# Performance work log

Hardware: AMD Instinct MI355X
Metric: run time of the kernel (lower is better)

The kernel has to match this reference:

```python
import jax, jax.numpy as jnp
import numpy as np

M, N, IN, H, NC = 2048, 64, 16, 256, 64
OUT = 3 * NC
NUM_LAYERS = 2


def _lstm_layer(x, Wih, Whh, bih, bhh):
    # x: (M, T, F); Wih: (4H, F); Whh: (4H, H). Torch gate order: i, f, g, o.
    xg = jnp.einsum('mtf,gf->mtg', x, Wih) + bih + bhh  # (M, T, 4H)
    h0 = jnp.zeros((x.shape[0], Whh.shape[1]), x.dtype)

    def step(carry, xt):
        h, c = carry
        gates = xt + h @ Whh.T
        i, f, g, o = jnp.split(gates, 4, axis=-1)
        c = jax.nn.sigmoid(f) * c + jax.nn.sigmoid(i) * jnp.tanh(g)
        h = jax.nn.sigmoid(o) * jnp.tanh(c)
        return (h, c), h

    (_, _), hs = jax.lax.scan(step, (h0, h0), jnp.swapaxes(xg, 0, 1))
    return jnp.swapaxes(hs, 0, 1)  # (M, T, H)


def setup_inputs() -> dict:
    key = jax.random.key(0)
    ks = jax.random.split(key, 12)
    s = 1.0 / np.sqrt(H)
    d = {
        'z': jax.random.normal(ks[0], (M, N, IN), jnp.float32),
        'Wih0': jax.random.normal(ks[1], (4 * H, IN), jnp.float32) * s,
        'Whh0': jax.random.normal(ks[2], (4 * H, H), jnp.float32) * s,
        'bih0': jax.random.normal(ks[3], (4 * H,), jnp.float32) * s,
        'bhh0': jax.random.normal(ks[4], (4 * H,), jnp.float32) * s,
        'Wih1': jax.random.normal(ks[5], (4 * H, H), jnp.float32) * s,
        'Whh1': jax.random.normal(ks[6], (4 * H, H), jnp.float32) * s,
        'bih1': jax.random.normal(ks[7], (4 * H,), jnp.float32) * s,
        'bhh1': jax.random.normal(ks[8], (4 * H,), jnp.float32) * s,
        'fcW': jax.random.normal(ks[9], (OUT, H), jnp.float32) * 0.02,
        'fcb': jax.random.normal(ks[10], (OUT,), jnp.float32) * 0.02,
    }
    return d


def reference(z, Wih0, Whh0, bih0, bhh0, Wih1, Whh1, bih1, bhh1, fcW, fcb):
    h = _lstm_layer(z, Wih0, Whh0, bih0, bhh0)
    h = _lstm_layer(h, Wih1, Whh1, bih1, bhh1)
    y = jnp.einsum('mth,oh->mto', h, fcW) + fcb  # (M, N, 3*NC)

    gammas = jax.nn.softmax(y[..., :NC], axis=2)
    sigmas = jnp.exp(y[..., NC:2 * NC])
    mus = y[..., 2 * NC:]

    key = jax.random.key(42)
    k1, k2 = jax.random.split(key)
    idx = jax.random.categorical(k1, jnp.log(gammas), axis=-1)  # (M, N)
    chosen_mu = jnp.take_along_axis(mus, idx[..., None], axis=2)     # (M, N, 1)
    chosen_sig = jnp.take_along_axis(sigmas, idx[..., None], axis=2)
    eps = jax.random.normal(k2, chosen_mu.shape, jnp.float32)
    x_pred = jax.lax.stop_gradient(chosen_mu + chosen_sig * eps)  # Normal.sample (no grad)

    kern_exp = (x_pred - mus) ** 2                         # broadcast repeat over NC
    kernels = jnp.exp(-0.5 * kern_exp) / sigmas ** 2
    kernels = kernels / ((2.0 * jnp.pi) ** (N / 2) * sigmas ** N)
    x_cond_prob = jnp.einsum('mtc,mtc->mt', gammas, kernels)  # (M, N)
    return x_pred, x_cond_prob
```

## Files before the change

kernel.cpp:

```cpp
#include <hip/hip_runtime.h>
#include <stdint.h>
#include <stddef.h>

#define Mdim 2048
#define Tdim 64
#define INdim 16
#define Hdim 256
#define NCdim 64
#define NUG 64
#define HSLAB (256 * 2048)
#define RSLOTS 16

typedef __attribute__((ext_vector_type(8))) short s16x8;
typedef __attribute__((ext_vector_type(4))) float f32x4;

#define PANEL_US (3 * 16 * 8 * 512)
#define SPOFF 65536
#define BFRAG_US (3 * 8 * 3 * 512)

#define OFF_BFRAG 0
#define OFF_WZ    1179648
#define OFF_BB    (OFF_WZ + 64 * 256)
#define OFF_WFCP  (OFF_BB + 64 * 32)
#define OFF_H0P   (OFF_WFCP + 256 * 64 * 4)
#define OFF_C0    (OFF_H0P + 1572864)
#define OFF_C1    (OFF_C0 + HSLAB)
#define OFF_RINGF (OFF_C1 + HSLAB)
#define OFF_Y     (OFF_RINGF + 12582912)
#define OFF_FCB3  (OFF_Y + RSLOTS * HSLAB)
#define WS_TOT    (OFF_FCB3 + 73728)

#define ROTL32(v, s) (((v) << (s)) | ((v) >> (32 - (s))))

__host__ __device__ inline void tf2x32(uint32_t k0, uint32_t k1, uint32_t x0, uint32_t x1,
                                       uint32_t* o0, uint32_t* o1) {
  uint32_t ks2 = k0 ^ k1 ^ 0x1BD11BDAu;
  x0 += k0; x1 += k1;
  x0 += x1; x1 = ROTL32(x1, 13); x1 ^= x0;
  x0 += x1; x1 = ROTL32(x1, 15); x1 ^= x0;
  x0 += x1; x1 = ROTL32(x1, 26); x1 ^= x0;
  x0 += x1; x1 = ROTL32(x1, 6);  x1 ^= x0;
  x0 += k1; x1 += ks2 + 1u;
  x0 += x1; x1 = ROTL32(x1, 17); x1 ^= x0;
  x0 += x1; x1 = ROTL32(x1, 29); x1 ^= x0;
  x0 += x1; x1 = ROTL32(x1, 16); x1 ^= x0;
  x0 += x1; x1 = ROTL32(x1, 24); x1 ^= x0;
  x0 += ks2; x1 += k0 + 2u;
  x0 += x1; x1 = ROTL32(x1, 13); x1 ^= x0;
  x0 += x1; x1 = ROTL32(x1, 15); x1 ^= x0;
  x0 += x1; x1 = ROTL32(x1, 26); x1 ^= x0;
  x0 += x1; x1 = ROTL32(x1, 6);  x1 ^= x0;
  x0 += k0; x1 += k1 + 3u;
  x0 += x1; x1 = ROTL32(x1, 17); x1 ^= x0;
  x0 += x1; x1 = ROTL32(x1, 29); x1 ^= x0;
  x0 += x1; x1 = ROTL32(x1, 16); x1 ^= x0;
  x0 += x1; x1 = ROTL32(x1, 24); x1 ^= x0;
  x0 += k1; x1 += ks2 + 4u;
  x0 += x1; x1 = ROTL32(x1, 13); x1 ^= x0;
  x0 += x1; x1 = ROTL32(x1, 15); x1 ^= x0;
  x0 += x1; x1 = ROTL32(x1, 26); x1 ^= x0;
  x0 += x1; x1 = ROTL32(x1, 6);  x1 ^= x0;
  x0 += ks2; x1 += k0 + 5u;
  *o0 = x0; *o1 = x1;
// ... 121 lines not shown
    unsigned short s2 = bf16_trunc(r1 - bf16_tof(s1));
    size_t base = ((size_t)(ug * 3 + cls) * 8 + kt) * (3 * 512) + pos;
    BF[base] = s0;
    BF[base + 512] = s1;
    BF[base + 1024] = s2;
  }
  for (int i = i0; i < 64 * 256; i += n) {
    int ug = i >> 8, k = (i >> 4) & 15, g = i & 15;
    int gd = (g & 3) * 256 + ug * 4 + (g >> 2);
    ws[OFF_WZ + i] = Wih0[gd * INdim + k];
  }
  for (int i = i0; i < 64 * 32; i += n) {
    int ug = i >> 5, r = i & 31, g = r & 15;
    int gd = (g & 3) * 256 + ug * 4 + (g >> 2);
    ws[OFF_BB + i] = (r < 16) ? (bih0[gd] + bhh0[gd]) : (bih1[gd] + bhh1[gd]);
  }
  unsigned short* BFC = (unsigned short*)(ws + OFF_FCB3);
  for (int i = i0; i < 12 * 8 * 512; i += n) {
    int ntkt = i >> 9, pos = i & 511;
    int nt = ntkt >> 3, kt = ntkt & 7;
    int l = pos >> 3, e = pos & 7;
    int c = nt * 16 + (l & 15);
    int k = kt * 32 + (l >> 4) * 8 + e;
    float w = fcW[c * Hdim + k];
    unsigned short s0 = bf16_trunc(w);
    float r1 = w - bf16_tof(s0);
    unsigned short s1 = bf16_trunc(r1);
    unsigned short s2 = bf16_trunc(r1 - bf16_tof(s1));
    size_t base = (size_t)ntkt * (3 * 512) + pos;
    BFC[base] = s0;
    BFC[base + 512] = s1;
    BFC[base + 1024] = s2;
  }
}

__device__ inline void cell1s(float gi, float gf, float gg, float go, float cold,
                              float* cn, float* hn) {
  float si = sigm_fast(gi), sf = sigm_fast(gf);
  float tg = fmaf(2.0f, sigm_fast(2.0f * gg), -1.0f);
  float so = sigm_fast(go);
  float cc = fmaf(sf, cold, si * tg);
  *cn = cc;
  *hn = so * fmaf(2.0f, sigm_fast(2.0f * cc), -1.0f);
}

#define GBS3 66

template <int MODE>
__launch_bounds__(512, 2)
__global__ void vfpg_step(const float* __restrict__ z, const float* __restrict__ ws,
                          float* __restrict__ wsm, int t) {
  __shared__ unsigned short lB01[2 * 2 * 8 * 2 * 512];
  __shared__ __align__(16) unsigned char uni[81920];
  __shared__ float lz[2 * 256];
  __shared__ float lbias[64];

  const int tid = threadIdx.x;
  const int rg = blockIdx.x & 7, ugc = blockIdx.x >> 3;
  const int mb = rg * 256;
  const int lane = tid & 63, wid = tid >> 6;
  float* gbuf = (float*)uni;

  {
    const unsigned short* BF = (const unsigned short*)(ws + OFF_BFRAG);
    const unsigned short* BG0 = BF + (size_t)(ugc * 2 + 0) * BFRAG_US;
    const unsigned short* BG1 = BF + (size_t)(ugc * 2 + 1) * BFRAG_US;
    for (int i = tid; i < 2 * 4608; i += 512) {
      int ugl = i / 4608;
      int r = i % 4608;
      int cls = r / 1536;
      int r2 = r % 1536;
      int kt = r2 / 192;
      int sp = (r2 / 64) % 3;
      int v = r2 & 63;
      const unsigned short* src = (ugl ? BG1 : BG0) + ((size_t)(cls * 8 + kt) * 3 + sp) * 512 + v * 8;
      s16x8 val = *(const s16x8*)src;
      if (cls < 2 && sp < 2) {
        ((s16x8*)lB01)[((((ugl * 2 + cls) * 8 + kt) * 2 + sp)) * 64 + v] = val;
      } else {
        int str = (cls == 2) ? (2 + sp) : cls;
        ((s16x8*)uni)[(((ugl * 5 + str) * 8 + kt)) * 64 + v] = val;
      }
    }
    if (tid < 128) ((float4*)lz)[tid] = ((const float4*)(ws + OFF_WZ + (ugc * 2) * 256))[tid];
    if (tid < 64) lbias[tid] = ws[OFF_BB + (ugc * 2) * 32 + tid];
  }
  __syncthreads();

  f32x4 aL0[2][2], aL1[2][2];
#pragma unroll
  for (int i = 0; i < 2; i++)
#pragma unroll
    for (int u = 0; u < 2; u++) { aL0[i][u] = (f32x4)0.0f; aL1[i][u] = (f32x4)0.0f; }

  if (MODE >= 1) {
    const unsigned short* p0 = (const unsigned short*)(ws + OFF_H0P) +
                               ((size_t)((t - 1) & 1) * 8 + rg) * PANEL_US;
    const unsigned short* p1 = (const unsigned short*)(ws + OFF_RINGF) +
                               ((size_t)((t - 2) & 15) * 8 + rg) * PANEL_US;
    const bool doH1 = (t >= 2);
    const s16x8* pL = (const s16x8*)lB01;
    const s16x8* pU = (const s16x8*)uni;

    s16x8 Ab0[6], Ab1[6];
    {
      size_t fb = ((size_t)(wid * 2) * 8 + 0) * 512 + lane * 8;
      Ab0[0] = *(const s16x8*)(p0 + fb);
      Ab0[1] = *(const s16x8*)(p0 + fb + SPOFF);
      Ab0[2] = *(const s16x8*)(p0 + fb + 2 * SPOFF);
      if (doH1) {
        Ab0[3] = *(const s16x8*)(p1 + fb);
        Ab0[4] = *(const s16x8*)(p1 + fb + SPOFF);
        Ab0[5] = *(const s16x8*)(p1 + fb + 2 * SPOFF);
      }
    }

#pragma unroll 1
    for (int kt = 0; kt < 8; kt++) {
      s16x8 bL0s0[2], bL0s1[2], bL0s2[2], bIs0[2], bIs1[2], bIs2[2], bHs0[2], bHs1[2], bHs2[2];
#pragma unroll
      for (int u = 0; u < 2; u++) {
        if (MODE == 1) {
          bL0s0[u] = pL[(((u * 2 + 0) * 8 + kt) * 2 + 0) * 64 + lane];
          bL0s1[u] = pL[(((u * 2 + 0) * 8 + kt) * 2 + 1) * 64 + lane];
          bL0s2[u] = pU[((u * 5 + 0) * 8 + kt) * 64 + lane];
        }
        bIs0[u] = pL[(((u * 2 + 1) * 8 + kt) * 2 + 0) * 64 + lane];
        bIs1[u] = pL[(((u * 2 + 1) * 8 + kt) * 2 + 1) * 64 + lane];
        bIs2[u] = pU[((u * 5 + 1) * 8 + kt) * 64 + lane];
        if (doH1) {
          bHs0[u] = pU[((u * 5 + 2) * 8 + kt) * 64 + lane];
          bHs1[u] = pU[((u * 5 + 3) * 8 + kt) * 64 + lane];
          bHs2[u] = pU[((u * 5 + 4) * 8 + kt) * 64 + lane];
        }
      }
#pragma unroll
      for (int i = 0; i < 2; i++) {
        s16x8* cur = (i & 1) ? Ab1 : Ab0;
        s16x8* nxt = (i & 1) ? Ab0 : Ab1;
        int nkt = (i < 1) ? kt : kt + 1;
        int ni = (i < 1) ? 1 : 0;
        if (nkt < 8) {
          size_t fb = ((size_t)(wid * 2 + ni) * 8 + nkt) * 512 + lane * 8;
          nxt[0] = *(const s16x8*)(p0 + fb);
          nxt[1] = *(const s16x8*)(p0 + fb + SPOFF);
          nxt[2] = *(const s16x8*)(p0 + fb + 2 * SPOFF);
          if (doH1) {
            nxt[3] = *(const s16x8*)(p1 + fb);
            nxt[4] = *(const s16x8*)(p1 + fb + SPOFF);
            nxt[5] = *(const s16x8*)(p1 + fb + 2 * SPOFF);
          }
        }
        s16x8 a0 = cur[0], a1 = cur[1], a2 = cur[2];
#pragma unroll
        for (int u = 0; u < 2; u++) {
          if (MODE == 1) {
            aL0[i][u] = __builtin_amdgcn_mfma_f32_16x16x32_bf16(a0, bL0s0[u], aL0[i][u], 0, 0, 0);
            aL0[i][u] = __builtin_amdgcn_mfma_f32_16x16x32_bf16(a0, bL0s1[u], aL0[i][u], 0, 0, 0);
            aL0[i][u] = __builtin_amdgcn_mfma_f32_16x16x32_bf16(a1, bL0s0[u], aL0[i][u], 0, 0, 0);
            aL0[i][u] = __builtin_amdgcn_mfma_f32_16x16x32_bf16(a1, bL0s1[u], aL0[i][u], 0, 0, 0);
            aL0[i][u] = __builtin_amdgcn_mfma_f32_16x16x32_bf16(a0, bL0s2[u], aL0[i][u], 0, 0, 0);
            aL0[i][u] = __builtin_amdgcn_mfma_f32_16x16x32_bf16(a2, bL0s0[u], aL0[i][u], 0, 0, 0);
          }
          aL1[i][u] = __builtin_amdgcn_mfma_f32_16x16x32_bf16(a0, bIs0[u], aL1[i][u], 0, 0, 0);
          aL1[i][u] = __builtin_amdgcn_mfma_f32_16x16x32_bf16(a0, bIs1[u], aL1[i][u], 0, 0, 0);
          aL1[i][u] = __builtin_amdgcn_mfma_f32_16x16x32_bf16(a1, bIs0[u], aL1[i][u], 0, 0, 0);
          aL1[i][u] = __builtin_amdgcn_mfma_f32_16x16x32_bf16(a1, bIs1[u], aL1[i][u], 0, 0, 0);
          aL1[i][u] = __builtin_amdgcn_mfma_f32_16x16x32_bf16(a0, bIs2[u], aL1[i][u], 0, 0, 0);
          aL1[i][u] = __builtin_amdgcn_mfma_f32_16x16x32_bf16(a2, bIs0[u], aL1[i][u], 0, 0, 0);
          if (doH1) {
            s16x8 c0 = cur[3], c1 = cur[4], c2 = cur[5];
            aL1[i][u] = __builtin_amdgcn_mfma_f32_16x16x32_bf16(c0, bHs0[u], aL1[i][u], 0, 0, 0);
            aL1[i][u] = __builtin_amdgcn_mfma_f32_16x16x32_bf16(c0, bHs1[u], aL1[i][u], 0, 0, 0);
            aL1[i][u] = __builtin_amdgcn_mfma_f32_16x16x32_bf16(c1, bHs0[u], aL1[i][u], 0, 0, 0);
            aL1[i][u] = __builtin_amdgcn_mfma_f32_16x16x32_bf16(c1, bHs1[u], aL1[i][u], 0, 0, 0);
            aL1[i][u] = __builtin_amdgcn_mfma_f32_16x16x32_bf16(c0, bHs2[u], aL1[i][u], 0, 0, 0);
            aL1[i][u] = __builtin_amdgcn_mfma_f32_16x16x32_bf16(c2, bHs0[u], aL1[i][u], 0, 0, 0);
          }
        }
      }
    }
  }
  __syncthreads();

  {
    int col = lane & 15, rb2 = (lane >> 4) * 4;
#pragma unroll
    for (int i = 0; i < 2; i++)
#pragma unroll
      for (int u = 0; u < 2; u++)
#pragma unroll
        for (int j = 0; j < 4; j++) {
          int row = (wid * 2 + i) * 16 + rb2 + j;
          if (MODE == 1) gbuf[row * GBS3 + u * 16 + col] = aL0[i][u][j];
          if (MODE >= 1) gbuf[row * GBS3 + 32 + u * 16 + col] = aL1[i][u][j];
        }
  }
  __syncthreads();

  float* c0w = wsm + OFF_C0;
  float* c1w = wsm + OFF_C1;
  const int ugl = tid >> 8;
  const int mloc = tid & 255;
  const int m = mb + mloc;
  const int ug = ugc * 2 + ugl;
  const int mtc = mloc >> 4, mrowc = mloc & 15;
  const int ktw = ug >> 3;
  const int lgw = (ug & 7) >> 1;
  const int ebase = (ug * 4) & 7;
  const int lww = lgw * 16 + mrowc;
  const size_t fo = ((size_t)mtc * 8 + ktw) * 512 + lww * 8 + ebase;

  if (MODE <= 1) {
    float zr[16];
#pragma unroll
    for (int f4 = 0; f4 < 4; f4++)
      *(float4*)&zr[f4 * 4] = *(const float4*)&z[(size_t)m * 1024 + t * 16 + f4 * 4];
    float g16[16];
#pragma unroll
    for (int gg = 0; gg < 16; gg++)
      g16[gg] = lbias[ugl * 32 + gg] + ((MODE == 1) ? gbuf[mloc * GBS3 + ugl * 16 + gg] : 0.0f);
    const float* lzu = lz + ugl * 256;
#pragma unroll
    for (int f = 0; f < 16; f++) {
      float zv = zr[f];
      float4 w0 = *(const float4*)&lzu[f * 16 + 0];
      float4 w1 = *(const float4*)&lzu[f * 16 + 4];
      float4 w2 = *(const float4*)&lzu[f * 16 + 8];
      float4 w3 = *(const float4*)&lzu[f * 16 + 12];
      g16[0] = fmaf(zv, w0.x, g16[0]);  g16[1] = fmaf(zv, w0.y, g16[1]);
      g16[2] = fmaf(zv, w0.z, g16[2]);  g16[3] = fmaf(zv, w0.w, g16[3]);
      g16[4] = fmaf(zv, w1.x, g16[4]);  g16[5] = fmaf(zv, w1.y, g16[5]);
      g16[6] = fmaf(zv, w1.z, g16[6]);  g16[7] = fmaf(zv, w1.w, g16[7]);
      g16[8] = fmaf(zv, w2.x, g16[8]);  g16[9] = fmaf(zv, w2.y, g16[9]);
      g16[10] = fmaf(zv, w2.z, g16[10]); g16[11] = fmaf(zv, w2.w, g16[11]);
      g16[12] = fmaf(zv, w3.x, g16[12]); g16[13] = fmaf(zv, w3.y, g16[13]);
      g16[14] = fmaf(zv, w3.z, g16[14]); g16[15] = fmaf(zv, w3.w, g16[15]);
    }
    unsigned short* wp = (unsigned short*)(wsm + OFF_H0P) +
                         ((size_t)(t & 1) * 8 + rg) * PANEL_US;
    short sp0[4], sp1[4], sp2[4];
#pragma unroll
    for (int ul = 0; ul < 4; ul++) {
      int u = ug * 4 + ul;
      size_t cidx = (size_t)u * 2048 + m;
      float cold = (MODE == 1) ? c0w[cidx] : 0.0f;
      float cn, hn;
      cell1s(g16[ul * 4 + 0], g16[ul * 4 + 1], g16[ul * 4 + 2], g16[ul * 4 + 3], cold, &cn, &hn);
      c0w[cidx] = cn;
      unsigned short s0 = bf16_trunc(hn);
      float r1 = hn - bf16_tof(s0);
      unsigned short s1 = bf16_trunc(r1);
      unsigned short s2 = bf16_trunc(r1 - bf16_tof(s1));
      sp0[ul] = (short)s0; sp1[ul] = (short)s1; sp2[ul] = (short)s2;
    }
    *(short4*)&wp[fo]             = make_short4(sp0[0], sp0[1], sp0[2], sp0[3]);
    *(short4*)&wp[fo + SPOFF]     = make_short4(sp1[0], sp1[1], sp1[2], sp1[3]);
    *(short4*)&wp[fo + 2 * SPOFF] = make_short4(sp2[0], sp2[1], sp2[2], sp2[3]);
  }

  if (MODE >= 1) {
    int slot = (t - 1) & 15;
    unsigned short* rp = (unsigned short*)(wsm + OFF_RINGF) +
                         ((size_t)slot * 8 + rg) * PANEL_US;
    short sp0[4], sp1[4], sp2[4];
#pragma unroll
    for (int ul = 0; ul < 4; ul++) {
      float gi = lbias[ugl * 32 + 16 + ul * 4 + 0] + gbuf[mloc * GBS3 + 32 + ugl * 16 + ul * 4 + 0];
      float gf = lbias[ugl * 32 + 16 + ul * 4 + 1] + gbuf[mloc * GBS3 + 32 + ugl * 16 + ul * 4 + 1];
      float gt = lbias[ugl * 32 + 16 + ul * 4 + 2] + gbuf[mloc * GBS3 + 32 + ugl * 16 + ul * 4 + 2];
      float go = lbias[ugl * 32 + 16 + ul * 4 + 3] + gbuf[mloc * GBS3 + 32 + ugl * 16 + ul * 4 + 3];
      int u = ug * 4 + ul;
      size_t cidx = (size_t)u * 2048 + m;
      float cold = (t >= 2) ? c1w[cidx] : 0.0f;
      float cn, hn;
      cell1s(gi, gf, gt, go, cold, &cn, &hn);
      c1w[cidx] = cn;
      unsigned short s0 = bf16_trunc(hn);
      float r1v = hn - bf16_tof(s0);
      unsigned short s1 = bf16_trunc(r1v);
      unsigned short s2 = bf16_trunc(r1v - bf16_tof(s1));
      sp0[ul] = (short)s0; sp1[ul] = (short)s1; sp2[ul] = (short)s2;
    }
    *(short4*)&rp[fo]             = make_short4(sp0[0], sp0[1], sp0[2], sp0[3]);
    *(short4*)&rp[fo + SPOFF]     = make_short4(sp1[0], sp1[1], sp1[2], sp1[3]);
    *(short4*)&rp[fo + 2 * SPOFF] = make_short4(sp2[0], sp2[1], sp2[2], sp2[3]);
  }
}

__launch_bounds__(512, 2)
__global__ void vfpg_fc(const float* __restrict__ ws, float* __restrict__ wsm) {
  const int tid = threadIdx.x;
  const int rg = blockIdx.x & 7;
  const int slot = (blockIdx.x >> 3) & 15;
  const int mtg = blockIdx.x >> 7;
  const int lane = tid & 63, wid = tid >> 6;
  const int mt = mtg * 8 + wid;

  const unsigned short* pa = (const unsigned short*)(ws + OFF_RINGF) +
                             ((size_t)slot * 8 + rg) * PANEL_US;
  const unsigned short* BFC = (const unsigned short*)(ws + OFF_FCB3);
  float* y = wsm + OFF_Y + (size_t)slot * (2048 * 192) + (size_t)(rg * 256) * 192;

  const int col = lane & 15, rb2 = (lane >> 4) * 4;

#pragma unroll 1
  for (int ng = 0; ng < 3; ng++) {
    f32x4 C[4];
#pragma unroll
    for (int j = 0; j < 4; j++) C[j] = (f32x4)0.0f;
#pragma unroll 1
    for (int kt = 0; kt < 8; kt++) {
      size_t fb = ((size_t)mt * 8 + kt) * 512 + lane * 8;
      s16x8 a0 = *(const s16x8*)(pa + fb);
      s16x8 a1 = *(const s16x8*)(pa + fb + SPOFF);
      s16x8 a2 = *(const s16x8*)(pa + fb + 2 * SPOFF);
#pragma unroll
      for (int n4 = 0; n4 < 4; n4++) {
        int nt = ng * 4 + n4;
        const unsigned short* bp = BFC + (size_t)(nt * 8 + kt) * (3 * 512) + lane * 8;
        s16x8 b0 = *(const s16x8*)(bp);
        s16x8 b1 = *(const s16x8*)(bp + 512);
        s16x8 b2 = *(const s16x8*)(bp + 1024);
        C[n4] = __builtin_amdgcn_mfma_f32_16x16x32_bf16(a0, b0, C[n4], 0, 0, 0);
        C[n4] = __builtin_amdgcn_mfma_f32_16x16x32_bf16(a0, b1, C[n4], 0, 0, 0);
        C[n4] = __builtin_amdgcn_mfma_f32_16x16x32_bf16(a1, b0, C[n4], 0, 0, 0);
        C[n4] = __builtin_amdgcn_mfma_f32_16x16x32_bf16(a1, b1, C[n4], 0, 0, 0);
        C[n4] = __builtin_amdgcn_mfma_f32_16x16x32_bf16(a0, b2, C[n4], 0, 0, 0);
        C[n4] = __builtin_amdgcn_mfma_f32_16x16x32_bf16(a2, b0, C[n4], 0, 0, 0);
      }
    }
#pragma unroll
    for (int n4 = 0; n4 < 4; n4++) {
      int c = (ng * 4 + n4) * 16 + col;
#pragma unroll
      for (int j = 0; j < 4; j++) {
        int mrow = mt * 16 + rb2 + j;
        y[(size_t)mrow * 192 + c] = C[n4][j];
      }
    }
  }
}

__launch_bounds__(512, 2)
__global__ void vfpg_samp(const float* __restrict__ ws, const float* __restrict__ fcb,
                          float* __restrict__ out, int tbase,
                          uint32_t k1a, uint32_t k1b, uint32_t k2a, uint32_t k2b) {
  const int tid = threadIdx.x;
  const int lane = tid & 63, wid = tid >> 6;
  const int ridx = blockIdx.x * 8 + wid;
  const int slot = ridx >> 11;
  const int m = ridx & 2047;

  const float* yrow = ws + OFF_Y + (size_t)ridx * 192;
  float yg = yrow[lane] + fcb[lane];
  float ys = yrow[64 + lane] + fcb[64 + lane];
  float ym = yrow[128 + lane] + fcb[128 + lane];

  uint32_t rid = (uint32_t)m * Tdim + (uint32_t)(tbase + slot);
  mdn_head(yg, ys, ym, lane, rid, k1a, k1b, k2a, k2b, out);
}

extern "C" void kernel_launch(void* const* d_in, const int* in_sizes, int n_in,
                              void* d_out, int out_size, void* d_ws, size_t ws_size,
                              hipStream_t stream) {
  const float* z    = (const float*)d_in[0];
  const float* Wih0 = (const float*)d_in[1];
  const float* Whh0 = (const float*)d_in[2];
  const float* bih0 = (const float*)d_in[3];
  const float* bhh0 = (const float*)d_in[4];
  const float* Wih1 = (const float*)d_in[5];
  const float* Whh1 = (const float*)d_in[6];
  const float* bih1 = (const float*)d_in[7];
  const float* bhh1 = (const float*)d_in[8];
  const float* fcW  = (const float*)d_in[9];
  const float* fcb  = (const float*)d_in[10];
  float* ws = (float*)d_ws;
  float* out = (float*)d_out;

  if (ws_size < (size_t)WS_TOT * sizeof(float)) return;

  vfpg_prep<<<dim3(512), dim3(256), 0, stream>>>(
      Wih0, Whh0, Wih1, Whh1, fcW, bih0, bhh0, bih1, bhh1, ws);

  uint32_t k1a, k1b, k2a, k2b;
  tf2x32(0u, 42u, 0u, 0u, &k1a, &k1b);
  tf2x32(0u, 42u, 0u, 1u, &k2a, &k2b);

  vfpg_step<0><<<dim3(256), dim3(512), 0, stream>>>(z, ws, ws, 0);
  for (int t = 1; t <= 63; t++) {
    vfpg_step<1><<<dim3(256), dim3(512), 0, stream>>>(z, ws, ws, t);
    if (t == 16 || t == 32 || t == 48) {
      vfpg_fc<<<dim3(256), dim3(512), 0, stream>>>(ws, ws);
      vfpg_samp<<<dim3(4096), dim3(512), 0, stream>>>(ws, fcb, out, t - 16,
                                                      k1a, k1b, k2a, k2b);
    }
  }
  vfpg_step<2><<<dim3(256), dim3(512), 0, stream>>>(z, ws, ws, 64);
  vfpg_fc<<<dim3(256), dim3(512), 0, stream>>>(ws, ws);
  vfpg_samp<<<dim3(4096), dim3(512), 0, stream>>>(ws, fcb, out, 48, k1a, k1b, k2a, k2b);
}
```

Measured before the change: 1.931 ms.

## Fuse per-timestep LSTM launches into one cooperative persistent kernel with barriers

Replaces the 65 step launches plus the periodic FC and sampling launches with one cooperative persistent kernel. It loops over all timesteps and synchronises each row group with an atomic-counter spin barrier in global memory. FC and the MDN head are folded into the step loop, and some weight fragments are now read from global memory each step instead of shared memory, freeing LDS. This removes launch overhead and per-launch LDS reloads, but adds spin-barrier cost, runs at one block per CU, and reads part of the B operands from cache instead of LDS.

After: 4.933 ms. 156% more time.

```diff
diff --git a/kernel.cpp b/kernel.cpp
--- a/kernel.cpp
+++ b/kernel.cpp
@@ -7,7 +7,6 @@
 #define INdim 16
 #define Hdim 256
 #define NCdim 64
-#define NUG 64
 #define HSLAB (256 * 2048)
 #define RSLOTS 16
 
@@ -28,7 +27,8 @@
 #define OFF_RINGF (OFF_C1 + HSLAB)
 #define OFF_Y     (OFF_RINGF + 12582912)
 #define OFF_FCB3  (OFF_Y + RSLOTS * HSLAB)
-#define WS_TOT    (OFF_FCB3 + 73728)
+#define OFF_SYNC  (OFF_FCB3 + 73728)
+#define WS_TOT    (OFF_SYNC + 128)
 
 #define ROTL32(v, s) (((v) << (s)) | ((v) >> (32 - (s))))
 
@@ -216,6 +216,7 @@
     BFC[base + 512] = s1;
     BFC[base + 1024] = s2;
   }
+  if (i0 < 128) ((unsigned int*)(ws + OFF_SYNC))[i0] = 0u;
 }
 
 __device__ inline void cell1s(float gi, float gf, float gg, float go, float cold,
@@ -230,12 +231,12 @@
 
 #define GBS3 66
 
-template <int MODE>
-__launch_bounds__(512, 2)
-__global__ void vfpg_step(const float* __restrict__ z, const float* __restrict__ ws,
-                          float* __restrict__ wsm, int t) {
+__launch_bounds__(512, 1)
+__global__ void vfpg_persist(const float* __restrict__ z, float* __restrict__ ws,
+                             const float* __restrict__ fcb, float* __restrict__ out,
+                             uint32_t k1a, uint32_t k1b, uint32_t k2a, uint32_t k2b) {
   __shared__ unsigned short lB01[2 * 2 * 8 * 2 * 512];
-  __shared__ __align__(16) unsigned char uni[81920];
+  __shared__ __align__(16) unsigned char uni[69632];
   __shared__ float lz[2 * 256];
   __shared__ float lbias[64];
 
@@ -244,305 +245,315 @@
   const int mb = rg * 256;
   const int lane = tid & 63, wid = tid >> 6;
   float* gbuf = (float*)uni;
-
-  {
-    const unsigned short* BF = (const unsigned short*)(ws + OFF_BFRAG);
-    const unsigned short* BG0 = BF + (size_t)(ugc * 2 + 0) * BFRAG_US;
-    const unsigned short* BG1 = BF + (size_t)(ugc * 2 + 1) * BFRAG_US;
-    for (int i = tid; i < 2 * 4608; i += 512) {
-      int ugl = i / 4608;
-      int r = i % 4608;
-      int cls = r / 1536;
-      int r2 = r % 1536;
-      int kt = r2 / 192;
-      int sp = (r2 / 64) % 3;
-      int v = r2 & 63;
-      const unsigned short* src = (ugl ? BG1 : BG0) + ((size_t)(cls * 8 + kt) * 3 + sp) * 512 + v * 8;
-      s16x8 val = *(const s16x8*)src;
-      if (cls < 2 && sp < 2) {
-        ((s16x8*)lB01)[((((ugl * 2 + cls) * 8 + kt) * 2 + sp)) * 64 + v] = val;
-      } else {
-        int str = (cls == 2) ? (2 + sp) : cls;
-        ((s16x8*)uni)[(((ugl * 5 + str) * 8 + kt)) * 64 + v] = val;
-      }
-    }
-    if (tid < 128) ((float4*)lz)[tid] = ((const float4*)(ws + OFF_WZ + (ugc * 2) * 256))[tid];
-    if (tid < 64) lbias[tid] = ws[OFF_BB + (ugc * 2) * 32 + tid];
-  }
+  unsigned int* sc = (unsigned int*)(ws + OFF_SYNC) + rg * 16;
+
+  const unsigned short* BF = (const unsigned short*)(ws + OFF_BFRAG);
+  const unsigned short* BG2[2] = {BF + (size_t)(ugc * 2 + 0) * BFRAG_US,
+                                  BF + (size_t)(ugc * 2 + 1) * BFRAG_US};
+
+  for (int i = tid; i < 2 * 2 * 8 * 2 * 64; i += 512) {
+    int ugl = i >> 11;
+    int r = i & 2047;
+    int cls = r >> 10;
+    int kt = (r >> 7) & 7;
+    int sp = (r >> 6) & 1;
+    int v = r & 63;
+    ((s16x8*)lB01)[(((ugl * 2 + cls) * 8 + kt) * 2 + sp) * 64 + v] =
+        *(const s16x8*)(BG2[ugl] + ((size_t)(cls * 8 + kt) * 3 + sp) * 512 + v * 8);
+  }
+  if (tid < 128) ((float4*)lz)[tid] = ((const float4*)(ws + OFF_WZ + (ugc * 2) * 256))[tid];
+  if (tid < 64) lbias[tid] = ws[OFF_BB + (ugc * 2) * 32 + tid];
   __syncthreads();
 
-  f32x4 aL0[2][2], aL1[2][2];
-#pragma unroll
-  for (int i = 0; i < 2; i++)
-#pragma unroll
-    for (int u = 0; u < 2; u++) { aL0[i][u] = (f32x4)0.0f; aL1[i][u] = (f32x4)0.0f; }
-
-  if (MODE >= 1) {
-    const unsigned short* p0 = (const unsigned short*)(ws + OFF_H0P) +
-                               ((size_t)((t - 1) & 1) * 8 + rg) * PANEL_US;
-    const unsigned short* p1 = (const unsigned short*)(ws + OFF_RINGF) +
-                               ((size_t)((t - 2) & 15) * 8 + rg) * PANEL_US;
+  float* c0w = ws + OFF_C0;
+  float* c1w = ws + OFF_C1;
+  const int ugl_c = tid >> 8;
+  const int mloc = tid & 255;
+  const int m = mb + mloc;
+  const int ug_c = ugc * 2 + ugl_c;
+  const int mtc = mloc >> 4, mrowc = mloc & 15;
+  const int ktw = ug_c >> 3;
+  const int lgw = (ug_c & 7) >> 1;
+  const int ebase = (ug_c * 4) & 7;
+  const int lww = lgw * 16 + mrowc;
+  const size_t fo = ((size_t)mtc * 8 + ktw) * 512 + lww * 8 + ebase;
+  const int fc_slot = ugc >> 1, fc_mhalf = ugc & 1;
+
+  unsigned int bcount = 0;
+
+#pragma unroll 1
+  for (int t = 0; t <= Tdim; t++) {
+    const bool doL0 = (t < Tdim);
+    const bool doL1 = (t >= 1);
     const bool doH1 = (t >= 2);
-    const s16x8* pL = (const s16x8*)lB01;
-    const s16x8* pU = (const s16x8*)uni;
-
-    s16x8 Ab0[6], Ab1[6];
-    {
-      size_t fb = ((size_t)(wid * 2) * 8 + 0) * 512 + lane * 8;
-      Ab0[0] = *(const s16x8*)(p0 + fb);
-      Ab0[1] = *(const s16x8*)(p0 + fb + SPOFF);
-      Ab0[2] = *(const s16x8*)(p0 + fb + 2 * SPOFF);
-      if (doH1) {
-        Ab0[3] = *(const s16x8*)(p1 + fb);
-        Ab0[4] = *(const s16x8*)(p1 + fb + SPOFF);
-        Ab0[5] = *(const s16x8*)(p1 + fb + 2 * SPOFF);
-      }
-    }
+
+    f32x4 aL0[2][2], aL1[2][2];
+#pragma unroll
+    for (int i = 0; i < 2; i++)
+#pragma unroll
+      for (int u = 0; u < 2; u++) { aL0[i][u] = (f32x4)0.0f; aL1[i][u] = (f32x4)0.0f; }
+
+    if (t >= 1) {
+      const unsigned short* p0 = (const unsigned short*)(ws + OFF_H0P) +
+                                 ((size_t)((t - 1) & 1) * 8 + rg) * PANEL_US;
+      const unsigned short* p1 = (const unsigned short*)(ws + OFF_RINGF) +
+                                 ((size_t)((t - 2) & 15) * 8 + rg) * PANEL_US;
+      const s16x8* pL = (const s16x8*)lB01;
+
+      s16x8 Ab0[6], Ab1[6];
+      {
+        size_t fb = ((size_t)(wid * 2) * 8 + 0) * 512 + lane * 8;
+        Ab0[0] = *(const s16x8*)(p0 + fb);
+        Ab0[1] = *(const s16x8*)(p0 + fb + SPOFF);
+        Ab0[2] = *(const s16x8*)(p0 + fb + 2 * SPOFF);
+        if (doH1) {
+          Ab0[3] = *(const s16x8*)(p1 + fb);
+          Ab0[4] = *(const s16x8*)(p1 + fb + SPOFF);
+          Ab0[5] = *(const s16x8*)(p1 + fb + 2 * SPOFF);
+        }
+      }
 
 #pragma unroll 1
-    for (int kt = 0; kt < 8; kt++) {
-      s16x8 bL0s0[2], bL0s1[2], bL0s2[2], bIs0[2], bIs1[2], bIs2[2], bHs0[2], bHs1[2], bHs2[2];
-#pragma unroll
-      for (int u = 0; u < 2; u++) {
-        if (MODE == 1) {
-          bL0s0[u] = pL[(((u * 2 + 0) * 8 + kt) * 2 + 0) * 64 + lane];
-          bL0s1[u] = pL[(((u * 2 + 0) * 8 + kt) * 2 + 1) * 64 + lane];
-          bL0s2[u] = pU[((u * 5 + 0) * 8 + kt) * 64 + lane];
-        }
-        bIs0[u] = pL[(((u * 2 + 1) * 8 + kt) * 2 + 0) * 64 + lane];
-        bIs1[u] = pL[(((u * 2 + 1) * 8 + kt) * 2 + 1) * 64 + lane];
-        bIs2[u] = pU[((u * 5 + 1) * 8 + kt) * 64 + lane];
-        if (doH1) {
-          bHs0[u] = pU[((u * 5 + 2) * 8 + kt) * 64 + lane];
-          bHs1[u] = pU[((u * 5 + 3) * 8 + kt) * 64 + lane];
-          bHs2[u] = pU[((u * 5 + 4) * 8 + kt) * 64 + lane];
-        }
-      }
-#pragma unroll
-      for (int i = 0; i < 2; i++) {
-        s16x8* cur = (i & 1) ? Ab1 : Ab0;
-        s16x8* nxt = (i & 1) ? Ab0 : Ab1;
-        int nkt = (i < 1) ? kt : kt + 1;
-        int ni = (i < 1) ? 1 : 0;
-        if (nkt < 8) {
-          size_t fb = ((size_t)(wid * 2 + ni) * 8 + nkt) * 512 + lane * 8;
-          nxt[0] = *(const s16x8*)(p0 + fb);
-          nxt[1] = *(const s16x8*)(p0 + fb + SPOFF);
-          nxt[2] = *(const s16x8*)(p0 + fb + 2 * SPOFF);
+      for (int kt = 0; kt < 8; kt++) {
+        s16x8 bL0s0[2], bL0s1[2], bL0s2[2], bIs0[2], bIs1[2], bIs2[2], bHs0[2], bHs1[2], bHs2[2];
+#pragma unroll
+        for (int u = 0; u < 2; u++) {
+          if (doL0) {
+            bL0s0[u] = pL[(((u * 2 + 0) * 8 + kt) * 2 + 0) * 64 + lane];
+            bL0s1[u] = pL[(((u * 2 + 0) * 8 + kt) * 2 + 1) * 64 + lane];
+            bL0s2[u] = *(const s16x8*)(BG2[u] + ((size_t)(0 * 8 + kt) * 3 + 2) * 512 + lane * 8);
+          }
+          bIs0[u] = pL[(((u * 2 + 1) * 8 + kt) * 2 + 0) * 64 + lane];
+          bIs1[u] = pL[(((u * 2 + 1) * 8 + kt) * 2 + 1) * 64 + lane];
+          bIs2[u] = *(const s16x8*)(BG2[u] + ((size_t)(1 * 8 + kt) * 3 + 2) * 512 + lane * 8);
           if (doH1) {
-            nxt[3] = *(const s16x8*)(p1 + fb);
-            nxt[4] = *(const s16x8*)(p1 + fb + SPOFF);
-            nxt[5] = *(const s16x8*)(p1 + fb + 2 * SPOFF);
+            bHs0[u] = *(const s16x8*)(BG2[u] + ((size_t)(2 * 8 + kt) * 3 + 0) * 512 + lane * 8);
+            bHs1[u] = *(const s16x8*)(BG2[u] + ((size_t)(2 * 8 + kt) * 3 + 1) * 512 + lane * 8);
+            bHs2[u] = *(const s16x8*)(BG2[u] + ((size_t)(2 * 8 + kt) * 3 + 2) * 512 + lane * 8);
           }
         }
-        s16x8 a0 = cur[0], a1 = cur[1], a2 = cur[2];
-#pragma unroll
-        for (int u = 0; u < 2; u++) {
-          if (MODE == 1) {
-            aL0[i][u] = __builtin_amdgcn_mfma_f32_16x16x32_bf16(a0, bL0s0[u], aL0[i][u], 0, 0, 0);
-            aL0[i][u] = __builtin_amdgcn_mfma_f32_16x16x32_bf16(a0, bL0s1[u], aL0[i][u], 0, 0, 0);
-            aL0[i][u] = __builtin_amdgcn_mfma_f32_16x16x32_bf16(a1, bL0s0[u], aL0[i][u], 0, 0, 0);
-            aL0[i][u] = __builtin_amdgcn_mfma_f32_16x16x32_bf16(a1, bL0s1[u], aL0[i][u], 0, 0, 0);
-            aL0[i][u] = __builtin_amdgcn_mfma_f32_16x16x32_bf16(a0, bL0s2[u], aL0[i][u], 0, 0, 0);
-            aL0[i][u] = __builtin_amdgcn_mfma_f32_16x16x32_bf16(a2, bL0s0[u], aL0[i][u], 0, 0, 0);
+#pragma unroll
+        for (int i = 0; i < 2; i++) {
+          s16x8* cur = (i & 1) ? Ab1 : Ab0;
+          s16x8* nxt = (i & 1) ? Ab0 : Ab1;
+          int nkt = (i < 1) ? kt : kt + 1;
+          int ni = (i < 1) ? 1 : 0;
+          if (nkt < 8) {
+            size_t fb = ((size_t)(wid * 2 + ni) * 8 + nkt) * 512 + lane * 8;
+            nxt[0] = *(const s16x8*)(p0 + fb);
+            nxt[1] = *(const s16x8*)(p0 + fb + SPOFF);
+            nxt[2] = *(const s16x8*)(p0 + fb + 2 * SPOFF);
+            if (doH1) {
+              nxt[3] = *(const s16x8*)(p1 + fb);
+              nxt[4] = *(const s16x8*)(p1 + fb + SPOFF);
+              nxt[5] = *(const s16x8*)(p1 + fb + 2 * SPOFF);
+            }
           }
-          aL1[i][u] = __builtin_amdgcn_mfma_f32_16x16x32_bf16(a0, bIs0[u], aL1[i][u], 0, 0, 0);
-          aL1[i][u] = __builtin_amdgcn_mfma_f32_16x16x32_bf16(a0, bIs1[u], aL1[i][u], 0, 0, 0);
-          aL1[i][u] = __builtin_amdgcn_mfma_f32_16x16x32_bf16(a1, bIs0[u], aL1[i][u], 0, 0, 0);
-          aL1[i][u] = __builtin_amdgcn_mfma_f32_16x16x32_bf16(a1, bIs1[u], aL1[i][u], 0, 0, 0);
-          aL1[i][u] = __builtin_amdgcn_mfma_f32_16x16x32_bf16(a0, bIs2[u], aL1[i][u], 0, 0, 0);
-          aL1[i][u] = __builtin_amdgcn_mfma_f32_16x16x32_bf16(a2, bIs0[u], aL1[i][u], 0, 0, 0);
-          if (doH1) {
-            s16x8 c0 = cur[3], c1 = cur[4], c2 = cur[5];
-            aL1[i][u] = __builtin_amdgcn_mfma_f32_16x16x32_bf16(c0, bHs0[u], aL1[i][u], 0, 0, 0);
-            aL1[i][u] = __builtin_amdgcn_mfma_f32_16x16x32_bf16(c0, bHs1[u], aL1[i][u], 0, 0, 0);
-            aL1[i][u] = __builtin_amdgcn_mfma_f32_16x16x32_bf16(c1, bHs0[u], aL1[i][u], 0, 0, 0);
-            aL1[i][u] = __builtin_amdgcn_mfma_f32_16x16x32_bf16(c1, bHs1[u], aL1[i][u], 0, 0, 0);
-            aL1[i][u] = __builtin_amdgcn_mfma_f32_16x16x32_bf16(c0, bHs2[u], aL1[i][u], 0, 0, 0);
-            aL1[i][u] = __builtin_amdgcn_mfma_f32_16x16x32_bf16(c2, bHs0[u], aL1[i][u], 0, 0, 0);
+          s16x8 a0 = cur[0], a1 = cur[1], a2 = cur[2];
+#pragma unroll
+          for (int u = 0; u < 2; u++) {
+            if (doL0) {
+              aL0[i][u] = __builtin_amdgcn_mfma_f32_16x16x32_bf16(a0, bL0s0[u], aL0[i][u], 0, 0, 0);
+              aL0[i][u] = __builtin_amdgcn_mfma_f32_16x16x32_bf16(a0, bL0s1[u], aL0[i][u], 0, 0, 0);
+              aL0[i][u] = __builtin_amdgcn_mfma_f32_16x16x32_bf16(a1, bL0s0[u], aL0[i][u], 0, 0, 0);
+              aL0[i][u] = __builtin_amdgcn_mfma_f32_16x16x32_bf16(a1, bL0s1[u], aL0[i][u], 0, 0, 0);
+              aL0[i][u] = __builtin_amdgcn_mfma_f32_16x16x32_bf16(a0, bL0s2[u], aL0[i][u], 0, 0, 0);
+              aL0[i][u] = __builtin_amdgcn_mfma_f32_16x16x32_bf16(a2, bL0s0[u], aL0[i][u], 0, 0, 0);
+            }
+            aL1[i][u] = __builtin_amdgcn_mfma_f32_16x16x32_bf16(a0, bIs0[u], aL1[i][u], 0, 0, 0);
+            aL1[i][u] = __builtin_amdgcn_mfma_f32_16x16x32_bf16(a0, bIs1[u], aL1[i][u], 0, 0, 0);
+            aL1[i][u] = __builtin_amdgcn_mfma_f32_16x16x32_bf16(a1, bIs0[u], aL1[i][u], 0, 0, 0);
+            aL1[i][u] = __builtin_amdgcn_mfma_f32_16x16x32_bf16(a1, bIs1[u], aL1[i][u], 0, 0, 0);
+            aL1[i][u] = __builtin_amdgcn_mfma_f32_16x16x32_bf16(a0, bIs2[u], aL1[i][u], 0, 0, 0);
+            aL1[i][u] = __builtin_amdgcn_mfma_f32_16x16x32_bf16(a2, bIs0[u], aL1[i][u], 0, 0, 0);
+            if (doH1) {
+              s16x8 c0 = cur[3], c1 = cur[4], c2 = cur[5];
+              aL1[i][u] = __builtin_amdgcn_mfma_f32_16x16x32_bf16(c0, bHs0[u], aL1[i][u], 0, 0, 0);
+              aL1[i][u] = __builtin_amdgcn_mfma_f32_16x16x32_bf16(c0, bHs1[u], aL1[i][u], 0, 0, 0);
+              aL1[i][u] = __builtin_amdgcn_mfma_f32_16x16x32_bf16(c1, bHs0[u], aL1[i][u], 0, 0, 0);
+              aL1[i][u] = __builtin_amdgcn_mfma_f32_16x16x32_bf16(c1, bHs1[u], aL1[i][u], 0, 0, 0);
+              aL1[i][u] = __builtin_amdgcn_mfma_f32_16x16x32_bf16(c0, bHs2[u], aL1[i][u], 0, 0, 0);
+              aL1[i][u] = __builtin_amdgcn_mfma_f32_16x16x32_bf16(c2, bHs0[u], aL1[i][u], 0, 0, 0);
+            }
           }
         }
       }
+
+      {
+        int col = lane & 15, rb2 = (lane >> 4) * 4;
+#pragma unroll
+        for (int i = 0; i < 2; i++)
+#pragma unroll
+          for (int u = 0; u < 2; u++)
+#pragma unroll
+            for (int j = 0; j < 4; j++) {
+              int row = (wid * 2 + i) * 16 + rb2 + j;
+              if (doL0) gbuf[row * GBS3 + u * 16 + col] = aL0[i][u][j];
+              gbuf[row * GBS3 + 32 + u * 16 + col] = aL1[i][u][j];
+            }
+      }
     }
-  }
-  __syncthreads();
-
-  {
-    int col = lane & 15, rb2 = (lane >> 4) * 4;
-#pragma unroll
-    for (int i = 0; i < 2; i++)
-#pragma unroll
-      for (int u = 0; u < 2; u++)
-#pragma unroll
-        for (int j = 0; j < 4; j++) {
-          int row = (wid * 2 + i) * 16 + rb2 + j;
-          if (MODE == 1) gbuf[row * GBS3 + u * 16 + col] = aL0[i][u][j];
-          if (MODE >= 1) gbuf[row * GBS3 + 32 + u * 16 + col] = aL1[i][u][j];
+    __syncthreads();
+
+    if (doL0) {
+      float zr[16];
+#pragma unroll
+      for (int f4 = 0; f4 < 4; f4++)
+        *(float4*)&zr[f4 * 4] = *(const float4*)&z[(size_t)m * 1024 + t * 16 + f4 * 4];
+      float g16[16];
+#pragma unroll
+      for (int gg = 0; gg < 16; gg++)
+        g16[gg] = lbias[ugl_c * 32 + gg] + ((t >= 1) ? gbuf[mloc * GBS3 + ugl_c * 16 + gg] : 0.0f);
+      const float* lzu = lz + ugl_c * 256;
+#pragma unroll
+      for (int f = 0; f < 16; f++) {
+        float zv = zr[f];
+        float4 w0 = *(const float4*)&lzu[f * 16 + 0];
+        float4 w1 = *(const float4*)&lzu[f * 16 + 4];
+        float4 w2 = *(const float4*)&lzu[f * 16 + 8];
+        float4 w3 = *(const float4*)&lzu[f * 16 + 12];
+        g16[0] = fmaf(zv, w0.x, g16[0]);  g16[1] = fmaf(zv, w0.y, g16[1]);
+        g16[2] = fmaf(zv, w0.z, g16[2]);  g16[3] = fmaf(zv, w0.w, g16[3]);
+        g16[4] = fmaf(zv, w1.x, g16[4]);  g16[5] = fmaf(zv, w1.y, g16[5]);
+        g16[6] = fmaf(zv, w1.z, g16[6]);  g16[7] = fmaf(zv, w1.w, g16[7]);
+        g16[8] = fmaf(zv, w2.x, g16[8]);  g16[9] = fmaf(zv, w2.y, g16[9]);
+        g16[10] = fmaf(zv, w2.z, g16[10]); g16[11] = fmaf(zv, w2.w, g16[11]);
+        g16[12] = fmaf(zv, w3.x, g16[12]); g16[13] = fmaf(zv, w3.y, g16[13]);
+        g16[14] = fmaf(zv, w3.z, g16[14]); g16[15] = fmaf(zv, w3.w, g16[15]);
+      }
+      unsigned short* wp = (unsigned short*)(ws + OFF_H0P) +
+                           ((size_t)(t & 1) * 8 + rg) * PANEL_US;
+      short sp0[4], sp1[4], sp2[4];
+#pragma unroll
+      for (int ul = 0; ul < 4; ul++) {
+        int u = ug_c * 4 + ul;
+        size_t cidx = (size_t)u * 2048 + m;
+        float cold = (t >= 1) ? c0w[cidx] : 0.0f;
+        float cn, hn;
+        cell1s(g16[ul * 4 + 0], g16[ul * 4 + 1], g16[ul * 4 + 2], g16[ul * 4 + 3], cold, &cn, &hn);
+        c0w[cidx] = cn;
+        unsigned short s0 = bf16_trunc(hn);
+        float r1 = hn - bf16_tof(s0);
+        unsigned short s1 = bf16_trunc(r1);
+        unsigned short s2 = bf16_trunc(r1 - bf16_tof(s1));
+        sp0[ul] = (short)s0; sp1[ul] = (short)s1; sp2[ul] = (short)s2;
+      }
+      *(short4*)&wp[fo]             = make_short4(sp0[0], sp0[1], sp0[2], sp0[3]);
+      *(short4*)&wp[fo + SPOFF]     = make_short4(sp1[0], sp1[1], sp1[2], sp1[3]);
+      *(short4*)&wp[fo + 2 * SPOFF] = make_short4(sp2[0], sp2[1], sp2[2], sp2[3]);
+    }
+
+    if (doL1) {
+      int slot = (t - 1) & 15;
+      unsigned short* rp = (unsigned short*)(ws + OFF_RINGF) +
+                           ((size_t)slot * 8 + rg) * PANEL_US;
+      short sp0[4], sp1[4], sp2[4];
+#pragma unroll
+      for (int ul = 0; ul < 4; ul++) {
+        float gi = lbias[ugl_c * 32 + 16 + ul * 4 + 0] + gbuf[mloc * GBS3 + 32 + ugl_c * 16 + ul * 4 + 0];
+        float gf = lbias[ugl_c * 32 + 16 + ul * 4 + 1] + gbuf[mloc * GBS3 + 32 + ugl_c * 16 + ul * 4 + 1];
+        float gt = lbias[ugl_c * 32 + 16 + ul * 4 + 2] + gbuf[mloc * GBS3 + 32 + ugl_c * 16 + ul * 4 + 2];
+        float go = lbias[ugl_c * 32 + 16 + ul * 4 + 3] + gbuf[mloc * GBS3 + 32 + ugl_c * 16 + ul * 4 + 3];
+        int u = ug_c * 4 + ul;
+        size_t cidx = (size_t)u * 2048 + m;
+        float cold = (t >= 2) ? c1w[cidx] : 0.0f;
+        float cn, hn;
+        cell1s(gi, gf, gt, go, cold, &cn, &hn);
+        c1w[cidx] = cn;
+        unsigned short s0 = bf16_trunc(hn);
+        float r1v = hn - bf16_tof(s0);
+        unsigned short s1 = bf16_trunc(r1v);
+        unsigned short s2 = bf16_trunc(r1v - bf16_tof(s1));
+        sp0[ul] = (short)s0; sp1[ul] = (short)s1; sp2[ul] = (short)s2;
+      }
+      *(short4*)&rp[fo]             = make_short4(sp0[0], sp0[1], sp0[2], sp0[3]);
+      *(short4*)&rp[fo + SPOFF]     = make_short4(sp1[0], sp1[1], sp1[2], sp1[3]);
+      *(short4*)&rp[fo + 2 * SPOFF] = make_short4(sp2[0], sp2[1], sp2[2], sp2[3]);
+    }
+
+    bcount++;
+    __syncthreads();
+    if (tid == 0) {
+      __threadfence();
+      atomicAdd(sc, 1u);
+      unsigned int target = 32u * bcount;
+      while (atomicAdd(sc, 0u) < target) __builtin_amdgcn_s_sleep(8);
+      __threadfence();
+    }
+    __syncthreads();
+
+    if (t == 16 || t == 32 || t == 48 || t == 64) {
+      int tbase = t - 16;
+      const unsigned short* pa = (const unsigned short*)(ws + OFF_RINGF) +
+                                 ((size_t)fc_slot * 8 + rg) * PANEL_US;
+      const unsigned short* BFC = (const unsigned short*)(ws + OFF_FCB3);
+      float* yl = (float*)uni;
+      const int col16 = lane & 15, rb2 = (lane >> 4) * 4;
+      const int mtl = wid & 3, part = wid >> 2;
+
+#pragma unroll 1
+      for (int chunk = 0; chunk < 2; chunk++) {
+        int mt = fc_mhalf * 8 + chunk * 4 + mtl;
+        f32x4 C[6];
+#pragma unroll
+        for (int j = 0; j < 6; j++) C[j] = (f32x4)0.0f;
+#pragma unroll 1
+        for (int kt = 0; kt < 8; kt++) {
+          size_t fb = ((size_t)mt * 8 + kt) * 512 + lane * 8;
+          s16x8 a0 = *(const s16x8*)(pa + fb);
+          s16x8 a1 = *(const s16x8*)(pa + fb + SPOFF);
+          s16x8 a2 = *(const s16x8*)(pa + fb + 2 * SPOFF);
+#pragma unroll
+          for (int n6 = 0; n6 < 6; n6++) {
+            int nt = part * 6 + n6;
+            const unsigned short* bp = BFC + (size_t)(nt * 8 + kt) * (3 * 512) + lane * 8;
+            s16x8 b0 = *(const s16x8*)(bp);
+            s16x8 b1 = *(const s16x8*)(bp + 512);
+            s16x8 b2 = *(const s16x8*)(bp + 1024);
+            C[n6] = __builtin_amdgcn_mfma_f32_16x16x32_bf16(a0, b0, C[n6], 0, 0, 0);
+            C[n6] = __builtin_amdgcn_mfma_f32_16x16x32_bf16(a0, b1, C[n6], 0, 0, 0);
+            C[n6] = __builtin_amdgcn_mfma_f32_16x16x32_bf16(a1, b0, C[n6], 0, 0, 0);
+            C[n6] = __builtin_amdgcn_mfma_f32_16x16x32_bf16(a1, b1, C[n6], 0, 0, 0);
+            C[n6] = __builtin_amdgcn_mfma_f32_16x16x32_bf16(a0, b2, C[n6], 0, 0, 0);
+            C[n6] = __builtin_amdgcn_mfma_f32_16x16x32_bf16(a2, b0, C[n6], 0, 0, 0);
+          }
         }
-  }
-  __syncthreads();
-
-  float* c0w = wsm + OFF_C0;
-  float* c1w = wsm + OFF_C1;
-  const int ugl = tid >> 8;
-  const int mloc = tid & 255;
-  const int m = mb + mloc;
-  const int ug = ugc * 2 + ugl;
-  const int mtc = mloc >> 4, mrowc = mloc & 15;
-  const int ktw = ug >> 3;
-  const int lgw = (ug & 7) >> 1;
-  const int ebase = (ug * 4) & 7;
-  const int lww = lgw * 16 + mrowc;
-  const size_t fo = ((size_t)mtc * 8 + ktw) * 512 + lww * 8 + ebase;
-
-  if (MODE <= 1) {
-    float zr[16];
-#pragma unroll
-    for (int f4 = 0; f4 < 4; f4++)
-      *(float4*)&zr[f4 * 4] = *(const float4*)&z[(size_t)m * 1024 + t * 16 + f4 * 4];
-    float g16[16];
-#pragma unroll
-    for (int gg = 0; gg < 16; gg++)
-      g16[gg] = lbias[ugl * 32 + gg] + ((MODE == 1) ? gbuf[mloc * GBS3 + ugl * 16 + gg] : 0.0f);
-    const float* lzu = lz + ugl * 256;
-#pragma unroll
-    for (int f = 0; f < 16; f++) {
-      float zv = zr[f];
-      float4 w0 = *(const float4*)&lzu[f * 16 + 0];
-      float4 w1 = *(const float4*)&lzu[f * 16 + 4];
-      float4 w2 = *(const float4*)&lzu[f * 16 + 8];
-      float4 w3 = *(const float4*)&lzu[f * 16 + 12];
-      g16[0] = fmaf(zv, w0.x, g16[0]);  g16[1] = fmaf(zv, w0.y, g16[1]);
-      g16[2] = fmaf(zv, w0.z, g16[2]);  g16[3] = fmaf(zv, w0.w, g16[3]);
-      g16[4] = fmaf(zv, w1.x, g16[4]);  g16[5] = fmaf(zv, w1.y, g16[5]);
-      g16[6] = fmaf(zv, w1.z, g16[6]);  g16[7] = fmaf(zv, w1.w, g16[7]);
-      g16[8] = fmaf(zv, w2.x, g16[8]);  g16[9] = fmaf(zv, w2.y, g16[9]);
-      g16[10] = fmaf(zv, w2.z, g16[10]); g16[11] = fmaf(zv, w2.w, g16[11]);
-      g16[12] = fmaf(zv, w3.x, g16[12]); g16[13] = fmaf(zv, w3.y, g16[13]);
-      g16[14] = fmaf(zv, w3.z, g16[14]); g16[15] = fmaf(zv, w3.w, g16[15]);
+        __syncthreads();
+#pragma unroll
+        for (int n6 = 0; n6 < 6; n6++) {
+          int c = (part * 6 + n6) * 16 + col16;
+#pragma unroll
+          for (int j = 0; j < 4; j++) {
+            int rloc = mtl * 16 + rb2 + j;
+            yl[rloc * 200 + c] = C[n6][j];
+          }
+        }
+        __syncthreads();
+#pragma unroll 1
+        for (int r8 = 0; r8 < 8; r8++) {
+          int rloc = wid * 8 + r8;
+          int mrow = mb + fc_mhalf * 128 + chunk * 64 + rloc;
+          float yg = yl[rloc * 200 + lane] + fcb[lane];
+          float ys = yl[rloc * 200 + 64 + lane] + fcb[64 + lane];
+          float ym = yl[rloc * 200 + 128 + lane] + fcb[128 + lane];
+          uint32_t rid = (uint32_t)mrow * Tdim + (uint32_t)(tbase + fc_slot);
+          mdn_head(yg, ys, ym, lane, rid, k1a, k1b, k2a, k2b, out);
+        }
+        __syncthreads();
+      }
+
+      bcount++;
+      __syncthreads();
+      if (tid == 0) {
+        __threadfence();
+        atomicAdd(sc, 1u);
+        unsigned int target = 32u * bcount;
+        while (atomicAdd(sc, 0u) < target) __builtin_amdgcn_s_sleep(8);
+        __threadfence();
+      }
+      __syncthreads();
     }
-    unsigned short* wp = (unsigned short*)(wsm + OFF_H0P) +
-                         ((size_t)(t & 1) * 8 + rg) * PANEL_US;
-    short sp0[4], sp1[4], sp2[4];
-#pragma unroll
-    for (int ul = 0; ul < 4; ul++) {
-      int u = ug * 4 + ul;
-      size_t cidx = (size_t)u * 2048 + m;
-      float cold = (MODE == 1) ? c0w[cidx] : 0.0f;
-      float cn, hn;
-      cell1s(g16[ul * 4 + 0], g16[ul * 4 + 1], g16[ul * 4 + 2], g16[ul * 4 + 3], cold, &cn, &hn);
-      c0w[cidx] = cn;
-      unsigned short s0 = bf16_trunc(hn);
-      float r1 = hn - bf16_tof(s0);
-      unsigned short s1 = bf16_trunc(r1);
-      unsigned short s2 = bf16_trunc(r1 - bf16_tof(s1));
-      sp0[ul] = (short)s0; sp1[ul] = (short)s1; sp2[ul] = (short)s2;
-    }
-    *(short4*)&wp[fo]             = make_short4(sp0[0], sp0[1], sp0[2], sp0[3]);
-    *(short4*)&wp[fo + SPOFF]     = make_short4(sp1[0], sp1[1], sp1[2], sp1[3]);
-    *(short4*)&wp[fo + 2 * SPOFF] = make_short4(sp2[0], sp2[1], sp2[2], sp2[3]);
-  }
-
-  if (MODE >= 1) {
-    int slot = (t - 1) & 15;
-    unsigned short* rp = (unsigned short*)(wsm + OFF_RINGF) +
-                         ((size_t)slot * 8 + rg) * PANEL_US;
-    short sp0[4], sp1[4], sp2[4];
-#pragma unroll
-    for (int ul = 0; ul < 4; ul++) {
-      float gi = lbias[ugl * 32 + 16 + ul * 4 + 0] + gbuf[mloc * GBS3 + 32 + ugl * 16 + ul * 4 + 0];
-      float gf = lbias[ugl * 32 + 16 + ul * 4 + 1] + gbuf[mloc * GBS3 + 32 + ugl * 16 + ul * 4 + 1];
-      float gt = lbias[ugl * 32 + 16 + ul * 4 + 2] + gbuf[mloc * GBS3 + 32 + ugl * 16 + ul * 4 + 2];
-      float go = lbias[ugl * 32 + 16 + ul * 4 + 3] + gbuf[mloc * GBS3 + 32 + ugl * 16 + ul * 4 + 3];
-      int u = ug * 4 + ul;
-      size_t cidx = (size_t)u * 2048 + m;
-      float cold = (t >= 2) ? c1w[cidx] : 0.0f;
-      float cn, hn;
-      cell1s(gi, gf, gt, go, cold, &cn, &hn);
-      c1w[cidx] = cn;
-      unsigned short s0 = bf16_trunc(hn);
-      float r1v = hn - bf16_tof(s0);
-      unsigned short s1 = bf16_trunc(r1v);
-      unsigned short s2 = bf16_trunc(r1v - bf16_tof(s1));
-      sp0[ul] = (short)s0; sp1[ul] = (short)s1; sp2[ul] = (short)s2;
-    }
-    *(short4*)&rp[fo]             = make_short4(sp0[0], sp0[1], sp0[2], sp0[3]);
-    *(short4*)&rp[fo + SPOFF]     = make_short4(sp1[0], sp1[1], sp1[2], sp1[3]);
-    *(short4*)&rp[fo + 2 * SPOFF] = make_short4(sp2[0], sp2[1], sp2[2], sp2[3]);
-  }
-}
-
-__launch_bounds__(512, 2)
-__global__ void vfpg_fc(const float* __restrict__ ws, float* __restrict__ wsm) {
-  const int tid = threadIdx.x;
-  const int rg = blockIdx.x & 7;
-  const int slot = (blockIdx.x >> 3) & 15;
-  const int mtg = blockIdx.x >> 7;
-  const int lane = tid & 63, wid = tid >> 6;
-  const int mt = mtg * 8 + wid;
-
-  const unsigned short* pa = (const unsigned short*)(ws + OFF_RINGF) +
-                             ((size_t)slot * 8 + rg) * PANEL_US;
-  const unsigned short* BFC = (const unsigned short*)(ws + OFF_FCB3);
-  float* y = wsm + OFF_Y + (size_t)slot * (2048 * 192) + (size_t)(rg * 256) * 192;
-
-  const int col = lane & 15, rb2 = (lane >> 4) * 4;
-
-#pragma unroll 1
-  for (int ng = 0; ng < 3; ng++) {
-    f32x4 C[4];
-#pragma unroll
-    for (int j = 0; j < 4; j++) C[j] = (f32x4)0.0f;
-#pragma unroll 1
-    for (int kt = 0; kt < 8; kt++) {
-      size_t fb = ((size_t)mt * 8 + kt) * 512 + lane * 8;
-      s16x8 a0 = *(const s16x8*)(pa + fb);
-      s16x8 a1 = *(const s16x8*)(pa + fb + SPOFF);
-      s16x8 a2 = *(const s16x8*)(pa + fb + 2 * SPOFF);
-#pragma unroll
-      for (int n4 = 0; n4 < 4; n4++) {
-        int nt = ng * 4 + n4;
-        const unsigned short* bp = BFC + (size_t)(nt * 8 + kt) * (3 * 512) + lane * 8;
-        s16x8 b0 = *(const s16x8*)(bp);
-        s16x8 b1 = *(const s16x8*)(bp + 512);
-        s16x8 b2 = *(const s16x8*)(bp + 1024);
-        C[n4] = __builtin_amdgcn_mfma_f32_16x16x32_bf16(a0, b0, C[n4], 0, 0, 0);
-        C[n4] = __builtin_amdgcn_mfma_f32_16x16x32_bf16(a0, b1, C[n4], 0, 0, 0);
-        C[n4] = __builtin_amdgcn_mfma_f32_16x16x32_bf16(a1, b0, C[n4], 0, 0, 0);
-        C[n4] = __builtin_amdgcn_mfma_f32_16x16x32_bf16(a1, b1, C[n4], 0, 0, 0);
-        C[n4] = __builtin_amdgcn_mfma_f32_16x16x32_bf16(a0, b2, C[n4], 0, 0, 0);
-        C[n4] = __builtin_amdgcn_mfma_f32_16x16x32_bf16(a2, b0, C[n4], 0, 0, 0);
-      }
-    }
-#pragma unroll
-    for (int n4 = 0; n4 < 4; n4++) {
-      int c = (ng * 4 + n4) * 16 + col;
-#pragma unroll
-      for (int j = 0; j < 4; j++) {
-        int mrow = mt * 16 + rb2 + j;
-        y[(size_t)mrow * 192 + c] = C[n4][j];
-      }
-    }
-  }
-}
-
-__launch_bounds__(512, 2)
-__global__ void vfpg_samp(const float* __restrict__ ws, const float* __restrict__ fcb,
-                          float* __restrict__ out, int tbase,
-                          uint32_t k1a, uint32_t k1b, uint32_t k2a, uint32_t k2b) {
-  const int tid = threadIdx.x;
-  const int lane = tid & 63, wid = tid >> 6;
-  const int ridx = blockIdx.x * 8 + wid;
-  const int slot = ridx >> 11;
-  const int m = ridx & 2047;
-
-  const float* yrow = ws + OFF_Y + (size_t)ridx * 192;
-  float yg = yrow[lane] + fcb[lane];
-  float ys = yrow[64 + lane] + fcb[64 + lane];
-  float ym = yrow[128 + lane] + fcb[128 + lane];
-
-  uint32_t rid = (uint32_t)m * Tdim + (uint32_t)(tbase + slot);
-  mdn_head(yg, ys, ym, lane, rid, k1a, k1b, k2a, k2b, out);
+  }
 }
 
 extern "C" void kernel_launch(void* const* d_in, const int* in_sizes, int n_in,
@@ -571,16 +582,8 @@
   tf2x32(0u, 42u, 0u, 0u, &k1a, &k1b);
   tf2x32(0u, 42u, 0u, 1u, &k2a, &k2b);
 
-  vfpg_step<0><<<dim3(256), dim3(512), 0, stream>>>(z, ws, ws, 0);
-  for (int t = 1; t <= 63; t++) {
-    vfpg_step<1><<<dim3(256), dim3(512), 0, stream>>>(z, ws, ws, t);
-    if (t == 16 || t == 32 || t == 48) {
-      vfpg_fc<<<dim3(256), dim3(512), 0, stream>>>(ws, ws);
-      vfpg_samp<<<dim3(4096), dim3(512), 0, stream>>>(ws, fcb, out, t - 16,
-                                                      k1a, k1b, k2a, k2b);
-    }
-  }
-  vfpg_step<2><<<dim3(256), dim3(512), 0, stream>>>(z, ws, ws, 64);
-  vfpg_fc<<<dim3(256), dim3(512), 0, stream>>>(ws, ws);
-  vfpg_samp<<<dim3(4096), dim3(512), 0, stream>>>(ws, fcb, out, 48, k1a, k1b, k2a, k2b);
-}
+  void* args[] = {(void*)&z, (void*)&ws, (void*)&fcb, (void*)&out,
+                  (void*)&k1a, (void*)&k1b, (void*)&k2a, (void*)&k2b};
+  hipLaunchCooperativeKernel((const void*)vfpg_persist, dim3(256), dim3(512),
+                             args, 0, stream);
+}
```
